# Kernel optimization log

Hardware: AMD Instinct MI355X
Metric: run time of the kernel (lower is better)

The kernel has to match this reference:

```python
import jax, jax.numpy as jnp
import numpy as np

DIM = 512
N_PATCH = 1024
HEADS = 8
LN_EPS = 1e-5
NORM_EPS = 1e-12


def _layernorm(x, g, b):
    mu = jnp.mean(x, axis=-1, keepdims=True)
    var = jnp.mean(jnp.square(x - mu), axis=-1, keepdims=True)
    return (x - mu) * jax.lax.rsqrt(var + LN_EPS) * g + b


def _l2norm(x):
    # matches F.normalize(dim=-1): x / max(||x||, eps)
    n = jnp.sqrt(jnp.sum(jnp.square(x), axis=-1, keepdims=True))
    return x / jnp.maximum(n, NORM_EPS)


def _gelu(x):
    return jax.nn.gelu(x, approximate=False)


def _cosine_attn_branch(x, qkv_w, qkv_b, ln_g, ln_b, proj_w, proj_b, temperature):
    B, N, D = x.shape
    H = HEADS
    hd = D // H
    qkv = _layernorm(x @ qkv_w + qkv_b, ln_g, ln_b)          # [B,N,3D]
    q, k, v = jnp.split(qkv, 3, axis=-1)
    def to_heads(t):
        return t.reshape(B, N, H, hd).transpose(0, 2, 1, 3)  # [B,H,N,hd]
    q, k, v = to_heads(q), to_heads(k), to_heads(v)
    q = _l2norm(q)
    k = _l2norm(k)
    # temperature: [H,1,1] broadcasts over [B,H,N,N]
    attn = jnp.einsum('bhnd,bhmd->bhnm', q, k) * temperature
    attn = jax.nn.softmax(attn, axis=-1)
    out = jnp.einsum('bhnm,bhmd->bhnd', attn, v)
    out = out.transpose(0, 2, 1, 3).reshape(B, N, D)
    return out @ proj_w + proj_b


def setup_inputs() -> dict:
    key = jax.random.key(0)
    ks = iter(jax.random.split(key, 40))
    D = DIM
    def rn(shape, scale=0.02):
        return (jax.random.normal(next(ks), shape, dtype=jnp.float32) * scale)
    inp = {
        'hsi_tokens': jax.random.normal(next(ks), (8, N_PATCH, D), dtype=jnp.float32),
        'lidar_tokens': jax.random.normal(next(ks), (8, N_PATCH, D), dtype=jnp.float32),
        'temperature': jnp.ones((HEADS, 1, 1), dtype=jnp.float32),
        'sq_w': rn((D, 3 * D)), 'sq_b': jnp.zeros((3 * D,), jnp.float32),
        'sq_ln_g': jnp.ones((3 * D,), jnp.float32), 'sq_ln_b': jnp.zeros((3 * D,), jnp.float32),
        'sproj_w': rn((D, D)), 'sproj_b': jnp.zeros((D,), jnp.float32),
        'pq_w': rn((D, 3 * D)), 'pq_b': jnp.zeros((3 * D,), jnp.float32),
        'pq_ln_g': jnp.ones((3 * D,), jnp.float32), 'pq_ln_b': jnp.zeros((3 * D,), jnp.float32),
        'pproj_w': rn((D, D)), 'pproj_b': jnp.zeros((D,), jnp.float32),
        'vf_w1': rn((D, 2 * D)), 'vf_b1': jnp.zeros((2 * D,), jnp.float32),
        'vf_w2': rn((2 * D, D)), 'vf_b2': jnp.zeros((D,), jnp.float32),
        'ag_w1': rn((2 * D, D)), 'ag_b1': jnp.zeros((D,), jnp.float32),
        'ag_ln_g': jnp.ones((D,), jnp.float32), 'ag_ln_b': jnp.zeros((D,), jnp.float32),
        'ag_w2': rn((D, 3)), 'ag_b2': jnp.zeros((3,), jnp.float32),
        'fr_w1': rn((D, 2 * D)), 'fr_b1': jnp.zeros((2 * D,), jnp.float32),
        'fr_w2': rn((2 * D, D)), 'fr_b2': jnp.zeros((D,), jnp.float32),
        'alpha': jnp.ones((1,), jnp.float32),
        'beta': jnp.ones((1,), jnp.float32),
    }
    return inp


def reference(hsi_tokens, lidar_tokens, temperature,
              sq_w, sq_b, sq_ln_g, sq_ln_b, sproj_w, sproj_b,
              pq_w, pq_b, pq_ln_g, pq_ln_b, pproj_w, pproj_b,
              vf_w1, vf_b1, vf_w2, vf_b2,
              ag_w1, ag_b1, ag_ln_g, ag_ln_b, ag_w2, ag_b2,
              fr_w1, fr_b1, fr_w2, fr_b2, alpha, beta):
    B, N, D = hsi_tokens.shape
    out_spectral = _cosine_attn_branch(hsi_tokens, sq_w, sq_b, sq_ln_g, sq_ln_b,
                                       sproj_w, sproj_b, temperature)
    out_spatial = _cosine_attn_branch(lidar_tokens, pq_w, pq_b, pq_ln_g, pq_ln_b,
                                      pproj_w, pproj_b, temperature)
    # volumetric fusion MLP (dropout is identity in eval)
    s = out_spectral + out_spatial
    volumetric_feat = _gelu(s @ vf_w1 + vf_b1) @ vf_w2 + vf_b2
    # adaptive gating
    hsi_global = jnp.mean(out_spectral, axis=1)    # [B,D]
    lidar_global = jnp.mean(out_spatial, axis=1)   # [B,D]
    concat = jnp.concatenate([hsi_global, lidar_global], axis=-1)  # [B,2D]
    g = _gelu(_layernorm(concat @ ag_w1 + ag_b1, ag_ln_g, ag_ln_b))
    gate = jax.nn.softmax(g @ ag_w2 + ag_b2, axis=-1)  # [B,3]
    w_spec = gate[:, 0][:, None, None]
    w_spat = gate[:, 1][:, None, None]
    w_vol = gate[:, 2][:, None, None]
    fused = w_spec * out_spectral + w_spat * out_spatial + w_vol * volumetric_feat
    fused_recal = _gelu(fused @ fr_w1 + fr_b1) @ fr_w2 + fr_b2
    return fused + alpha * fused_recal + beta * (hsi_tokens + lidar_tokens) * 0.5
```

## Files before the change

### kernel.cpp

```cpp
#include <hip/hip_runtime.h>
#include <hip/hip_bf16.h>
#include <math.h>

#define B_   8
#define N_   1024
#define D_   512
#define H_   8
#define HD_  64
#define D3_  1536
#define M_   (B_ * N_)

#define WOFF_SQ    0
#define WOFF_PQ    786432
#define WOFF_SPROJ 1572864
#define WOFF_PPROJ 1835008
#define WOFF_VF1   2097152
#define WOFF_VF2   2621440
#define WOFF_FR1   3145728
#define WOFF_FR2   3670016

typedef float f32x4 __attribute__((ext_vector_type(4)));
typedef __bf16 bf16x8 __attribute__((ext_vector_type(8)));

union FragU {
    uint4 u4;
    unsigned int u[4];
    ushort s[8];
    bf16x8 v;
};

static __device__ __forceinline__ ushort f2bf(float x) {
    union { __bf16 h; ushort u; } c;
    c.h = (__bf16)x;
    return c.u;
}

static __device__ __forceinline__ float bf2f(ushort u) {
    union { unsigned u; float f; } c;
    c.u = ((unsigned)u) << 16;
    return c.f;
}

static __device__ __forceinline__ unsigned int pack2(float a, float b) {
    return (unsigned int)f2bf(a) | ((unsigned int)f2bf(b) << 16);
}

static __device__ __forceinline__ float gelu_f(float x) {
    return 0.5f * x * (1.0f + erff(x * 0.7071067811865475f));
}

#if __has_builtin(__builtin_amdgcn_exp2f)
static __device__ __forceinline__ float exp2_fast(float x) { return __builtin_amdgcn_exp2f(x); }
#else
static __device__ __forceinline__ float exp2_fast(float x) { return exp2f(x); }
#endif

static __device__ __forceinline__ void gload16(const ushort* g, ushort* lds) {
    __builtin_amdgcn_global_load_lds(
        (const __attribute__((address_space(1))) void*)g,
        (__attribute__((address_space(3))) void*)lds, 16, 0, 0);
}

static __device__ __forceinline__ float blk_sum(float v, float* red) {
    #pragma unroll
    for (int off = 32; off; off >>= 1) v += __shfl_xor(v, off);
    const int w = threadIdx.x >> 6;
    __syncthreads();
    if ((threadIdx.x & 63) == 0) red[w] = v;
    __syncthreads();
    return red[0] + red[1] + red[2] + red[3];
}

template <int BM, int BN, int ACT, int OUT, bool FINAL, bool GROUP>
__global__ __launch_bounds__(256) void pgemm_k(
    const ushort* __restrict__ A, const ushort* __restrict__ Wt,
    const ushort* __restrict__ Wt2, const float* __restrict__ bias,
    const float* __restrict__ bias2, int Msplit,
    void* __restrict__ Cv, int nbx, int Nn, int K,
    const ushort* __restrict__ fusedb, const ushort* __restrict__ resb,
    const float* __restrict__ alphap, const float* __restrict__ betap)
{
    constexpr int MI = BM / 32;
    constexpr int NJ = BN / 32;
    constexpr int CA = BM / 16;
    constexpr int CB = BN / 16;
    __shared__ ushort Asm[2][BM * 32];
    __shared__ ushort Bsm[2][BN * 32];
    const int tid = threadIdx.x;
    const int w = tid >> 6, l = tid & 63;
    const int cpx = gridDim.x >> 3;
    const int wg = (blockIdx.x & 7) * cpx + (blockIdx.x >> 3);
    const int m0 = (wg / nbx) * BM, n0 = (wg % nbx) * BN;
    const int wr = w >> 1, wc = w & 1;
    const int lr = l & 15, g = l >> 4;

    const ushort* W_ = (!GROUP || m0 < Msplit) ? Wt : Wt2;
    const float* b_ = (!GROUP || m0 < Msplit) ? bias : bias2;

    f32x4 acc[MI][NJ] = {};
    const int nt = K >> 5;

    #define STAGE(buf, kt)                                                        \
        do {                                                                      \
            const int k0s = (kt) << 5;                                            \
            for (int c = w; c < CA; c += 4)                                       \
                gload16(&A[(size_t)(m0 + c * 16 + lr) * K + k0s + 8 * g],         \
                        &Asm[buf][c * 512]);                                      \
            for (int c = w; c < CB; c += 4)                                       \
                gload16(&W_[(size_t)(n0 + c * 16 + lr) * K + k0s + 8 * g],        \
                        &Bsm[buf][c * 512]);                                      \
        } while (0)

    STAGE(0, 0);
    __syncthreads();
    int cur = 0;
    for (int t = 0; t < nt; ++t) {
        if (t + 1 < nt) STAGE(cur ^ 1, t + 1);
        FragU af[MI], bf4[NJ];
        #pragma unroll
        for (int mi = 0; mi < MI; ++mi)
            af[mi].u4 = *reinterpret_cast<const uint4*>(
                &Asm[cur][(wr * MI + mi) * 512 + l * 8]);
        #pragma unroll
        for (int nj = 0; nj < NJ; ++nj)
            bf4[nj].u4 = *reinterpret_cast<const uint4*>(
                &Bsm[cur][(wc * NJ + nj) * 512 + l * 8]);
        #pragma unroll
        for (int mi = 0; mi < MI; ++mi)
            #pragma unroll
            for (int nj = 0; nj < NJ; ++nj)
                acc[mi][nj] = __builtin_amdgcn_mfma_f32_16x16x32_bf16(
                    af[mi].v, bf4[nj].v, acc[mi][nj], 0, 0, 0);
        __syncthreads();
        cur ^= 1;
    }
    #undef STAGE

    float alpha = 0.f, beta = 0.f;
    if (FINAL) { alpha = alphap[0]; beta = betap[0]; }
    #pragma unroll
    for (int mi = 0; mi < MI; ++mi) {
        #pragma unroll
        for (int r = 0; r < 4; ++r) {
            const int m = m0 + wr * (MI * 16) + mi * 16 + g * 4 + r;
            #pragma unroll
            for (int nj = 0; nj < NJ; ++nj) {
                const int n = n0 + wc * (NJ * 16) + nj * 16 + lr;
                const size_t idx = (size_t)m * Nn + n;
                float v = acc[mi][nj][r] + b_[n];
                if (ACT == 1) v = gelu_f(v);
                if (FINAL)
                    v = bf2f(fusedb[idx]) + alpha * v + beta * bf2f(resb[idx]);
                if (OUT == 0) ((float*)Cv)[idx] = v;
                else          ((ushort*)Cv)[idx] = f2bf(v);
            }
        }
    }
}

__global__ __launch_bounds__(256) void cvtw_k(
    const float* __restrict__ w0, const float* __restrict__ w1,
    const float* __restrict__ w2, const float* __restrict__ w3,
    const float* __restrict__ w4, const float* __restrict__ w5,
    const float* __restrict__ w6, const float* __restrict__ w7,
    ushort* __restrict__ dst)
{
    __shared__ ushort T[64][72];
    const int id = blockIdx.z;
    int K, Nn, off;
    const float* src;
    switch (id) {
        case 0: src = w0; K = 512;  Nn = 1536; off = WOFF_SQ;    break;
        case 1: src = w1; K = 512;  Nn = 1536; off = WOFF_PQ;    break;
        case 2: src = w2; K = 512;  Nn = 512;  off = WOFF_SPROJ; break;
        case 3: src = w3; K = 512;  Nn = 512;  off = WOFF_PPROJ; break;
        case 4: src = w4; K = 512;  Nn = 1024; off = WOFF_VF1;   break;
        case 5: src = w5; K = 1024; Nn = 512;  off = WOFF_VF2;   break;
        case 6: src = w6; K = 512;  Nn = 1024; off = WOFF_FR1;   break;
        default: src = w7; K = 1024; Nn = 512; off = WOFF_FR2;   break;
    }
    const int n0 = blockIdx.x * 64, k0 = blockIdx.y * 64;
    if (n0 >= Nn || k0 >= K) return;
    const int t = threadIdx.x;
    const int q = t >> 6, e = t & 63;
    #pragma unroll 4
    for (int i = 0; i < 16; ++i) {
        const int kl = q * 16 + i;
        T[e][kl] = f2bf(src[(size_t)(k0 + kl) * Nn + n0 + e]);
    }
    __syncthreads();
    #pragma unroll 4
    for (int i = 0; i < 16; ++i) {
        const int nl = q * 16 + i;
        dst[(size_t)off + (size_t)(n0 + nl) * K + k0 + e] = T[nl][e];
    }
}

__global__ __launch_bounds__(256) void cvt3_k(const float* __restrict__ h,
                                              const float* __restrict__ l,
                                              ushort* __restrict__ xh,
                                              ushort* __restrict__ xl,
                                              ushort* __restrict__ rb)
{
    const size_t i = ((size_t)blockIdx.x * 256 + threadIdx.x) * 8;
    const float4 h0 = *reinterpret_cast<const float4*>(h + i);
    const float4 h1 = *reinterpret_cast<const float4*>(h + i + 4);
    const float4 l0 = *reinterpret_cast<const float4*>(l + i);
    const float4 l1 = *reinterpret_cast<const float4*>(l + i + 4);
    FragU oh, ol, orr;
    oh.u[0] = pack2(h0.x, h0.y); oh.u[1] = pack2(h0.z, h0.w);
    oh.u[2] = pack2(h1.x, h1.y); oh.u[3] = pack2(h1.z, h1.w);
    ol.u[0] = pack2(l0.x, l0.y); ol.u[1] = pack2(l0.z, l0.w);
    ol.u[2] = pack2(l1.x, l1.y); ol.u[3] = pack2(l1.z, l1.w);
    orr.u[0] = pack2(0.5f * (h0.x + l0.x), 0.5f * (h0.y + l0.y));
    orr.u[1] = pack2(0.5f * (h0.z + l0.z), 0.5f * (h0.w + l0.w));
    orr.u[2] = pack2(0.5f * (h1.x + l1.x), 0.5f * (h1.y + l1.y));
    orr.u[3] = pack2(0.5f * (h1.z + l1.z), 0.5f * (h1.w + l1.w));
    *reinterpret_cast<uint4*>(xh + i) = oh.u4;
    *reinterpret_cast<uint4*>(xl + i) = ol.u4;
    *reinterpret_cast<uint4*>(rb + i) = orr.u4;
}

__global__ __launch_bounds__(256) void cvtadd_k(const ushort* __restrict__ a,
                                                const ushort* __restrict__ b,
                                                ushort* __restrict__ dst)
{
    const size_t i = ((size_t)blockIdx.x * 256 + threadIdx.x) * 8;
    FragU x, y, o;
    x.u4 = *reinterpret_cast<const uint4*>(a + i);
    y.u4 = *reinterpret_cast<const uint4*>(b + i);
    #pragma unroll
    for (int e = 0; e < 8; ++e) o.s[e] = f2bf(bf2f(x.s[e]) + bf2f(y.s[e]));
    *reinterpret_cast<uint4*>(dst + i) = o.u4;
}

__global__ __launch_bounds__(256) void lnprep_k(ushort* __restrict__ x,
                                                const float* __restrict__ lng0,
                                                const float* __restrict__ lnb0,
                                                const float* __restrict__ lng1,
                                                const float* __restrict__ lnb1,
                                                const float* __restrict__ temp,
                                                ushort* __restrict__ Kb,
                                                ushort* __restrict__ Vt)
{
    __shared__ ushort Vs[8 * 512];
    const int w = threadIdx.x >> 6, l = threadIdx.x & 63;
    const int n0 = blockIdx.x * 8;
    const float L2E = 1.4426950408889634f;
    const float* lng = (n0 < 8192) ? lng0 : lng1;
    const float* lnb = (n0 < 8192) ? lnb0 : lnb1;

    #pragma unroll
    for (int rr = 0; rr < 2; ++rr) {
        const int row = n0 + w * 2 + rr;
        const int bb = row >> 10;
        const int n = row & 1023;
        ushort* xr = x + (size_t)row * D3_;
        float qv[24];
        #pragma unroll
        for (int i = 0; i < 24; ++i) qv[i] = bf2f(xr[l + 64 * i]);
        float s = 0.f, ss = 0.f;
        #pragma unroll
        for (int i = 0; i < 24; ++i) { s += qv[i]; ss += qv[i] * qv[i]; }
        #pragma unroll
        for (int off = 32; off; off >>= 1) {
            s += __shfl_xor(s, off);
            ss += __shfl_xor(ss, off);
        }
        const float mu = s * (1.0f / D3_);
        const float var = ss * (1.0f / D3_) - mu * mu;
        const float rs = rsqrtf(var + 1e-5f);
        #pragma unroll
        for (int i = 0; i < 24; ++i)
            qv[i] = (qv[i] - mu) * rs * lng[l + 64 * i] + lnb[l + 64 * i];
        float sq[16];
        #pragma unroll
        for (int i = 0; i < 16; ++i) sq[i] = qv[i] * qv[i];
        #pragma unroll
        for (int off = 32; off; off >>= 1)
            #pragma unroll
            for (int i = 0; i < 16; ++i) sq[i] += __shfl_xor(sq[i], off);
        #pragma unroll
        for (int i = 0; i < 8; ++i) {
            const float qs = temp[i] * L2E / fmaxf(sqrtf(sq[i]), 1e-12f);
            xr[i * 64 + l] = f2bf(qv[i] * qs);
        }
        #pragma unroll
        for (int i = 0; i < 8; ++i) {
            const float ks = 1.0f / fmaxf(sqrtf(sq[8 + i]), 1e-12f);
            Kb[((size_t)(bb * 8 + i) * N_ + n) * HD_ + l] = f2bf(qv[8 + i] * ks);
        }
        #pragma unroll
        for (int i = 0; i < 8; ++i)
            Vs[(w * 2 + rr) * 512 + i * 64 + l] = f2bf(qv[16 + i]);
    }
    __syncthreads();
    const int bb = n0 >> 10;
    #pragma unroll
    for (int it = 0; it < 2; ++it) {
        const int combo = threadIdx.x + it * 256;
        FragU f;
        #pragma unroll
        for (int tok = 0; tok < 8; ++tok) f.s[tok] = Vs[tok * 512 + combo];
        *reinterpret_cast<uint4*>(
            &Vt[((size_t)(bb * 8 + (combo >> 6)) * HD_ + (combo & 63)) * N_ + (n0 & 1023)]) = f.u4;
    }
}

__global__ __launch_bounds__(256) void fattn_k(const ushort* __restrict__ Qu,
                                               const ushort* __restrict__ Kb,
                                               const ushort* __restrict__ Vt,
                                               const float* __restrict__ temp,
                                               ushort* __restrict__ out)
{
    __shared__ ushort Ks[2][64 * 72];
    __shared__ ushort Vs[2][64 * 72];
    const int tid = threadIdx.x;
    const int cpx = gridDim.x >> 3;
    const int wg = (blockIdx.x & 7) * cpx + (blockIdx.x >> 3);
    const int nb = wg & 7;
    const int h  = (wg >> 3) & 7;
    const int bb = wg >> 6;
    const int bh = bb * 8 + h;
    const int n0 = nb * 128;
    const int w  = tid >> 6;
    const int l  = tid & 63;
    const int lr = l & 15;
    const int g  = l >> 4;
    const float m2 = fabsf(temp[h]) * 1.4426950408889634f;
    const f32x4 mInit = {-m2, -m2, -m2, -m2};

    FragU ones;
    ones.u[0] = ones.u[1] = ones.u[2] = ones.u[3] = 0x3F803F80u;

    const int qb = n0 + w * 32;
    FragU qa0, qa1, qb0, qb1;
    {
        const size_t rb0 = (size_t)(bb * N_ + qb + lr) * D3_ + h * 64 + 8 * g;
        const size_t rb1 = (size_t)(bb * N_ + qb + 16 + lr) * D3_ + h * 64 + 8 * g;
        qa0.u4 = *reinterpret_cast<const uint4*>(&Qu[rb0]);
        qa1.u4 = *reinterpret_cast<const uint4*>(&Qu[rb0 + 32]);
        qb0.u4 = *reinterpret_cast<const uint4*>(&Qu[rb1]);
        qb1.u4 = *reinterpret_cast<const uint4*>(&Qu[rb1 + 32]);
    }

    f32x4 OA[4] = {};
    f32x4 OB[4] = {};
    f32x4 LSA = {0.f, 0.f, 0.f, 0.f};
    f32x4 LSB = {0.f, 0.f, 0.f, 0.f};

    const ushort* kbase = Kb + (size_t)bh * N_ * HD_;
    const ushort* vbase = Vt + (size_t)bh * HD_ * N_;
    const int sr = tid >> 3;
    const int sc = (tid & 7) * 8;
    uint4 k0r, k1r, v0r, v1r;

    #define LOADT(kt)                                                           \
        do {                                                                    \
            const ushort* ks_ = kbase + (size_t)((kt) * 64) * HD_;              \
            const ushort* vs_ = vbase + (kt) * 64;                              \
            k0r = *reinterpret_cast<const uint4*>(ks_ + sr * HD_ + sc);         \
            k1r = *reinterpret_cast<const uint4*>(ks_ + (sr + 32) * HD_ + sc);  \
            v0r = *reinterpret_cast<const uint4*>(vs_ + (size_t)sr * N_ + sc);  \
            v1r = *reinterpret_cast<const uint4*>(vs_ + (size_t)(sr + 32) * N_ + sc); \
        } while (0)
    #define WRITET(p)                                                           \
        do {                                                                    \
            *reinterpret_cast<uint4*>(&Ks[p][sr * 72 + sc]) = k0r;              \
            *reinterpret_cast<uint4*>(&Ks[p][(sr + 32) * 72 + sc]) = k1r;       \
            *reinterpret_cast<uint4*>(&Vs[p][sr * 72 + sc]) = v0r;              \
            *reinterpret_cast<uint4*>(&Vs[p][(sr + 32) * 72 + sc]) = v1r;       \
        } while (0)

    LOADT(0);
    WRITET(0);

    #pragma unroll 1
    for (int kt = 0; kt < 16; ++kt) {
        const int p = kt & 1;
        __syncthreads();
        if (kt < 15) LOADT(kt + 1);

        unsigned paA[2][4], paB[2][4];
        #pragma unroll
        for (int j = 0; j < 4; ++j) {
            FragU ka, kc;
            ka.u4 = *reinterpret_cast<const uint4*>(&Ks[p][(j * 16 + lr) * 72 + 8 * g]);
            kc.u4 = *reinterpret_cast<const uint4*>(&Ks[p][(j * 16 + lr) * 72 + 32 + 8 * g]);
            f32x4 sA = mInit, sB = mInit;
            sA = __builtin_amdgcn_mfma_f32_16x16x32_bf16(ka.v, qa0.v, sA, 0, 0, 0);
            sA = __builtin_amdgcn_mfma_f32_16x16x32_bf16(kc.v, qa1.v, sA, 0, 0, 0);
            sB = __builtin_amdgcn_mfma_f32_16x16x32_bf16(ka.v, qb0.v, sB, 0, 0, 0);
            sB = __builtin_amdgcn_mfma_f32_16x16x32_bf16(kc.v, qb1.v, sB, 0, 0, 0);
            float pA[4], pB[4];
            #pragma unroll
            for (int r = 0; r < 4; ++r) {
                pA[r] = exp2_fast(sA[r]);
                pB[r] = exp2_fast(sB[r]);
            }
            paA[j >> 1][2 * (j & 1) + 0] = pack2(pA[0], pA[1]);
            paA[j >> 1][2 * (j & 1) + 1] = pack2(pA[2], pA[3]);
            paB[j >> 1][2 * (j & 1) + 0] = pack2(pB[0], pB[1]);
            paB[j >> 1][2 * (j & 1) + 1] = pack2(pB[2], pB[3]);
        }

        __builtin_amdgcn_s_setprio(1);
        #pragma unroll
        for (int ks = 0; ks < 2; ++ks) {
            FragU fa, fb2;
            fa.u[0] = paA[ks][0]; fa.u[1] = paA[ks][1];
            fa.u[2] = paA[ks][2]; fa.u[3] = paA[ks][3];
            fb2.u[0] = paB[ks][0]; fb2.u[1] = paB[ks][1];
            fb2.u[2] = paB[ks][2]; fb2.u[3] = paB[ks][3];
            LSA = __builtin_amdgcn_mfma_f32_16x16x32_bf16(fa.v, ones.v, LSA, 0, 0, 0);
            LSB = __builtin_amdgcn_mfma_f32_16x16x32_bf16(fb2.v, ones.v, LSB, 0, 0, 0);
            #pragma unroll
            for (int s4 = 0; s4 < 4; ++s4) {
                FragU vb;
                const int vi = (lr + 16 * s4) * 72 + ks * 32 + 4 * g;
                *reinterpret_cast<uint2*>(&vb.u[0]) =
                    *reinterpret_cast<const uint2*>(&Vs[p][vi]);
                *reinterpret_cast<uint2*>(&vb.u[2]) =
                    *reinterpret_cast<const uint2*>(&Vs[p][vi + 16]);
                OA[s4] = __builtin_amdgcn_mfma_f32_16x16x32_bf16(fa.v, vb.v, OA[s4], 0, 0, 0);
                OB[s4] = __builtin_amdgcn_mfma_f32_16x16x32_bf16(fb2.v, vb.v, OB[s4], 0, 0, 0);
            }
        }
        __builtin_amdgcn_s_setprio(0);

        if (kt < 15) WRITET(p ^ 1);
    }
    #undef LOADT
    #undef WRITET

    ushort* outp = out + ((size_t)(bb * N_) + qb) * D_ + h * HD_;
    #pragma unroll
    for (int r = 0; r < 4; ++r) {
        const float iA = 1.0f / LSA[r];
        const float iB = 1.0f / LSB[r];
        ushort* rowA = outp + (size_t)(4 * g + r) * D_;
        ushort* rowB = outp + (size_t)(16 + 4 * g + r) * D_;
        #pragma unroll
        for (int s4 = 0; s4 < 4; ++s4) {
            rowA[s4 * 16 + lr] = f2bf(OA[s4][r] * iA);
            rowB[s4 * 16 + lr] = f2bf(OB[s4][r] * iB);
        }
    }
}

__global__ __launch_bounds__(256) void means_k(const ushort* __restrict__ spec,
                                               const ushort* __restrict__ spat,
                                               float* __restrict__ Gp)
{
    const int b = blockIdx.x >> 5;
    const int ch = blockIdx.x & 31;
    const int n0 = ch * 32;
    const int d0 = threadIdx.x * 2;
    float s1a = 0.f, s1b = 0.f, s2a = 0.f, s2b = 0.f;
    #pragma unroll 4
    for (int n = 0; n < 32; ++n) {
        const size_t idx = ((size_t)(b * N_) + n0 + n) * D_ + d0;
        ushort u1[2], u2[2];
        *reinterpret_cast<unsigned*>(u1) = *reinterpret_cast<const unsigned*>(spec + idx);
        *reinterpret_cast<unsigned*>(u2) = *reinterpret_cast<const unsigned*>(spat + idx);
        s1a += bf2f(u1[0]); s1b += bf2f(u1[1]);
        s2a += bf2f(u2[0]); s2b += bf2f(u2[1]);
    }
    float* gp = Gp + (size_t)blockIdx.x * 1024;
    gp[d0] = s1a; gp[d0 + 1] = s1b;
    gp[512 + d0] = s2a; gp[512 + d0 + 1] = s2b;
}

__global__ __launch_bounds__(256) void gate1_k(const float* __restrict__ Gp,
                                               const float* __restrict__ w1,
                                               const float* __restrict__ b1,
                                               float* __restrict__ y)
{
    __shared__ float xs[1024];
    __shared__ float red[4][64];
    const int jc = blockIdx.x, b = blockIdx.y, tid = threadIdx.x;
    for (int k = tid; k < 1024; k += 256) {
        float s = 0.f;
        #pragma unroll 8
        for (int c = 0; c < 32; ++c) s += Gp[(size_t)(b * 32 + c) * 1024 + k];
        xs[k] = s * (1.0f / N_);
    }
    __syncthreads();
    const int jl = tid & 63;
    const int jj = jc * 64 + jl;
    const int seg = tid >> 6;
    float acc = 0.f;
    const float* wp = w1 + (size_t)(seg * 256) * 512 + jj;
    const float* xp = xs + seg * 256;
    #pragma unroll 8
    for (int k = 0; k < 256; ++k) acc += xp[k] * wp[(size_t)k * 512];
    red[seg][jl] = acc;
    __syncthreads();
    if (tid < 64)
        y[b * 512 + jc * 64 + tid] =
            red[0][tid] + red[1][tid] + red[2][tid] + red[3][tid] + b1[jc * 64 + tid];
}

__global__ __launch_bounds__(256) void gate2_k(const float* __restrict__ y,
                                               const float* __restrict__ lng,
                                               const float* __restrict__ lnb,
                                               const float* __restrict__ w2,
                                               const float* __restrict__ b2,
                                               float* __restrict__ gate)
{
    __shared__ float red[4];
    const int b = blockIdx.x, tid = threadIdx.x;
    const float v0 = y[b * 512 + tid];
    const float v1 = y[b * 512 + 256 + tid];
    const float s = blk_sum(v0 + v1, red);
    const float ss = blk_sum(v0 * v0 + v1 * v1, red);
    const float mu = s * (1.0f / 512.0f);
    const float var = ss * (1.0f / 512.0f) - mu * mu;
    const float rs = rsqrtf(var + 1e-5f);
    const float z0 = gelu_f((v0 - mu) * rs * lng[tid] + lnb[tid]);
    const float z1 = gelu_f((v1 - mu) * rs * lng[tid + 256] + lnb[tid + 256]);
    float p0 = z0 * w2[tid * 3 + 0] + z1 * w2[(tid + 256) * 3 + 0];
    float p1 = z0 * w2[tid * 3 + 1] + z1 * w2[(tid + 256) * 3 + 1];
    float p2 = z0 * w2[tid * 3 + 2] + z1 * w2[(tid + 256) * 3 + 2];
    p0 = blk_sum(p0, red);
    p1 = blk_sum(p1, red);
    p2 = blk_sum(p2, red);
    if (tid == 0) {
        p0 += b2[0]; p1 += b2[1]; p2 += b2[2];
        const float m = fmaxf(p0, fmaxf(p1, p2));
        const float e0 = expf(p0 - m), e1 = expf(p1 - m), e2 = expf(p2 - m);
        const float inv = 1.0f / (e0 + e1 + e2);
        gate[b * 3 + 0] = e0 * inv;
        gate[b * 3 + 1] = e1 * inv;
        gate[b * 3 + 2] = e2 * inv;
    }
}

__global__ __launch_bounds__(256) void fuse_k(
    const ushort* __restrict__ spec, const ushort* __restrict__ spat,
    const ushort* __restrict__ volb, const float* __restrict__ gate,
    ushort* __restrict__ fb)
{
    const size_t i4 = ((size_t)blockIdx.x * 256 + threadIdx.x) * 4;
    const int b = (int)(i4 >> 19);
    const float g0 = gate[b * 3 + 0], g1 = gate[b * 3 + 1], g2 = gate[b * 3 + 2];
    ushort au[4], cu[4], vu[4];
    *reinterpret_cast<uint2*>(au) = *reinterpret_cast<const uint2*>(spec + i4);
    *reinterpret_cast<uint2*>(cu) = *reinterpret_cast<const uint2*>(spat + i4);
    *reinterpret_cast<uint2*>(vu) = *reinterpret_cast<const uint2*>(volb + i4);
    union { ushort s[4]; uint2 u; } ob;
    #pragma unroll
    for (int e = 0; e < 4; ++e)
        ob.s[e] = f2bf(g0 * bf2f(au[e]) + g1 * bf2f(cu[e]) + g2 * bf2f(vu[e]));
    *reinterpret_cast<uint2*>(fb + i4) = ob.u;
}

extern "C" void kernel_launch(void* const* d_in, const int* in_sizes, int n_in,
                              void* d_out, int out_size, void* d_ws, size_t ws_size,
                              hipStream_t stream)
{
    const float* hsi    = (const float*)d_in[0];
    const float* lidar  = (const float*)d_in[1];
    const float* temp   = (const float*)d_in[2];
    const float* sq_w   = (const float*)d_in[3];
    const float* sq_b   = (const float*)d_in[4];
    const float* sq_lng = (const float*)d_in[5];
    const float* sq_lnb = (const float*)d_in[6];
    const float* sproj_w = (const float*)d_in[7];
    const float* sproj_b = (const float*)d_in[8];
    const float* pq_w   = (const float*)d_in[9];
    const float* pq_b   = (const float*)d_in[10];
    const float* pq_lng = (const float*)d_in[11];
    const float* pq_lnb = (const float*)d_in[12];
    const float* pproj_w = (const float*)d_in[13];
    const float* pproj_b = (const float*)d_in[14];
    const float* vf_w1  = (const float*)d_in[15];
    const float* vf_b1  = (const float*)d_in[16];
    const float* vf_w2  = (const float*)d_in[17];
    const float* vf_b2  = (const float*)d_in[18];
    const float* ag_w1  = (const float*)d_in[19];
    const float* ag_b1  = (const float*)d_in[20];
    const float* ag_lng = (const float*)d_in[21];
    const float* ag_lnb = (const float*)d_in[22];
    const float* ag_w2  = (const float*)d_in[23];
    const float* ag_b2  = (const float*)d_in[24];
    const float* fr_w1  = (const float*)d_in[25];
    const float* fr_b1  = (const float*)d_in[26];
    const float* fr_w2  = (const float*)d_in[27];
    const float* fr_b2  = (const float*)d_in[28];
    const float* alpha  = (const float*)d_in[29];
    const float* beta   = (const float*)d_in[30];
    float* out = (float*)d_out;

    ushort* base = (ushort*)d_ws;
    ushort* Qkv  = base;
    ushort* Ob   = base;
    ushort* Sb   = base + 8388608;
    ushort* volb = base + 12582912;
    ushort* fb   = base + 16777216;
    float*  Gp   = (float*)(base + 20971520);
    float*  gate = Gp + 262144;
    float*  ybuf = gate + 64;
    ushort* Kb   = base + 25165824;
    ushort* Vt   = base + 33554432;
    ushort* Hb   = base + 25165824;
    ushort* Ab   = base + 41943040;
    ushort* Xb   = base + 41943040;
    ushort* Wb   = base + 50331648;
    ushort* Rb   = base + 54525952;

    const dim3 blk(256);

    cvtw_k<<<dim3(24, 16, 8), blk, 0, stream>>>(sq_w, pq_w, sproj_w, pproj_w,
                                                vf_w1, vf_w2, fr_w1, fr_w2, Wb);
    cvt3_k<<<2048, blk, 0, stream>>>(hsi, lidar, Xb, Xb + (size_t)M_ * D_, Rb);

    pgemm_k<128,128,0,1,false,true><<<1536, blk, 0, stream>>>(
        Xb, Wb + WOFF_SQ, Wb + WOFF_PQ, sq_b, pq_b, M_,
        Qkv, 12, D3_, D_, nullptr, nullptr, nullptr, nullptr);

    lnprep_k<<<2048, blk, 0, stream>>>(Qkv, sq_lng, sq_lnb, pq_lng, pq_lnb,
                                       temp, Kb, Vt);

    fattn_k<<<1024, blk, 0, stream>>>(Qkv, Kb, Vt, temp, Ab);

    pgemm_k<128,64,0,1,false,true><<<1024, blk, 0, stream>>>(
        Ab, Wb + WOFF_SPROJ, Wb + WOFF_PPROJ, sproj_b, pproj_b, M_,
        Ob, 8, D_, D_, nullptr, nullptr, nullptr, nullptr);

    const ushort* spec_b = Ob;
    const ushort* spat_b = Ob + (size_t)M_ * D_;

    means_k<<<256, blk, 0, stream>>>(spec_b, spat_b, Gp);
    gate1_k<<<dim3(8, 8), blk, 0, stream>>>(Gp, ag_w1, ag_b1, ybuf);
    gate2_k<<<B_, blk, 0, stream>>>(ybuf, ag_lng, ag_lnb, ag_w2, ag_b2, gate);

    cvtadd_k<<<2048, blk, 0, stream>>>(spec_b, spat_b, Sb);
    pgemm_k<128,64,1,1,false,false><<<1024, blk, 0, stream>>>(
        Sb, Wb + WOFF_VF1, nullptr, vf_b1, nullptr, 0,
        Hb, 16, 1024, D_, nullptr, nullptr, nullptr, nullptr);
    pgemm_k<128,64,0,1,false,false><<<512, blk, 0, stream>>>(
        Hb, Wb + WOFF_VF2, nullptr, vf_b2, nullptr, 0,
        volb, 8, D_, 1024, nullptr, nullptr, nullptr, nullptr);

    fuse_k<<<4096, blk, 0, stream>>>(spec_b, spat_b, volb, gate, fb);
    pgemm_k<128,64,1,1,false,false><<<1024, blk, 0, stream>>>(
        fb, Wb + WOFF_FR1, nullptr, fr_b1, nullptr, 0,
        Hb, 16, 1024, D_, nullptr, nullptr, nullptr, nullptr);
    pgemm_k<128,64,0,0,true,false><<<512, blk, 0, stream>>>(
        Hb, Wb + WOFF_FR2, nullptr, fr_b2, nullptr, 0,
        out, 8, D_, 1024, fb, Rb, alpha, beta);
}
```

Before: 350.2 us.

## Load K/V fragments directly from global in flash attention, enlarge QKV GEMM tile

The flash attention kernel no longer stages K and V tiles through double-buffered shared memory with barriers. Each wave now reads its MFMA operand fragments straight from global memory and relies on the L1/L2 caches for reuse across the four waves. This removes LDS traffic and __syncthreads, but the loads are no longer software-prefetched, so latency can be exposed and global/cache traffic rises. Separately, the QKV projection GEMM tile grows from 128 to 256 rows and the grid shrinks to match.

```diff
diff --git a/kernel.cpp b/kernel.cpp
--- a/kernel.cpp
+++ b/kernel.cpp
@@ -313,8 +313,6 @@
                                                const float* __restrict__ temp,
                                                ushort* __restrict__ out)
 {
-    __shared__ ushort Ks[2][64 * 72];
-    __shared__ ushort Vs[2][64 * 72];
     const int tid = threadIdx.x;
     const int cpx = gridDim.x >> 3;
     const int wg = (blockIdx.x & 7) * cpx + (blockIdx.x >> 3);
@@ -351,42 +349,16 @@
 
     const ushort* kbase = Kb + (size_t)bh * N_ * HD_;
     const ushort* vbase = Vt + (size_t)bh * HD_ * N_;
-    const int sr = tid >> 3;
-    const int sc = (tid & 7) * 8;
-    uint4 k0r, k1r, v0r, v1r;
-
-    #define LOADT(kt)                                                           \
-        do {                                                                    \
-            const ushort* ks_ = kbase + (size_t)((kt) * 64) * HD_;              \
-            const ushort* vs_ = vbase + (kt) * 64;                              \
-            k0r = *reinterpret_cast<const uint4*>(ks_ + sr * HD_ + sc);         \
-            k1r = *reinterpret_cast<const uint4*>(ks_ + (sr + 32) * HD_ + sc);  \
-            v0r = *reinterpret_cast<const uint4*>(vs_ + (size_t)sr * N_ + sc);  \
-            v1r = *reinterpret_cast<const uint4*>(vs_ + (size_t)(sr + 32) * N_ + sc); \
-        } while (0)
-    #define WRITET(p)                                                           \
-        do {                                                                    \
-            *reinterpret_cast<uint4*>(&Ks[p][sr * 72 + sc]) = k0r;              \
-            *reinterpret_cast<uint4*>(&Ks[p][(sr + 32) * 72 + sc]) = k1r;       \
-            *reinterpret_cast<uint4*>(&Vs[p][sr * 72 + sc]) = v0r;              \
-            *reinterpret_cast<uint4*>(&Vs[p][(sr + 32) * 72 + sc]) = v1r;       \
-        } while (0)
-
-    LOADT(0);
-    WRITET(0);
 
     #pragma unroll 1
     for (int kt = 0; kt < 16; ++kt) {
-        const int p = kt & 1;
-        __syncthreads();
-        if (kt < 15) LOADT(kt + 1);
-
         unsigned paA[2][4], paB[2][4];
         #pragma unroll
         for (int j = 0; j < 4; ++j) {
+            const ushort* krow = kbase + (size_t)(kt * 64 + j * 16 + lr) * HD_ + 8 * g;
             FragU ka, kc;
-            ka.u4 = *reinterpret_cast<const uint4*>(&Ks[p][(j * 16 + lr) * 72 + 8 * g]);
-            kc.u4 = *reinterpret_cast<const uint4*>(&Ks[p][(j * 16 + lr) * 72 + 32 + 8 * g]);
+            ka.u4 = *reinterpret_cast<const uint4*>(krow);
+            kc.u4 = *reinterpret_cast<const uint4*>(krow + 32);
             f32x4 sA = mInit, sB = mInit;
             sA = __builtin_amdgcn_mfma_f32_16x16x32_bf16(ka.v, qa0.v, sA, 0, 0, 0);
             sA = __builtin_amdgcn_mfma_f32_16x16x32_bf16(kc.v, qa1.v, sA, 0, 0, 0);
@@ -416,22 +388,19 @@
             LSB = __builtin_amdgcn_mfma_f32_16x16x32_bf16(fb2.v, ones.v, LSB, 0, 0, 0);
             #pragma unroll
             for (int s4 = 0; s4 < 4; ++s4) {
+                const ushort* vrow = vbase + (size_t)(lr + 16 * s4) * N_
+                                     + kt * 64 + ks * 32 + 4 * g;
                 FragU vb;
-                const int vi = (lr + 16 * s4) * 72 + ks * 32 + 4 * g;
                 *reinterpret_cast<uint2*>(&vb.u[0]) =
-                    *reinterpret_cast<const uint2*>(&Vs[p][vi]);
+                    *reinterpret_cast<const uint2*>(vrow);
                 *reinterpret_cast<uint2*>(&vb.u[2]) =
-                    *reinterpret_cast<const uint2*>(&Vs[p][vi + 16]);
+                    *reinterpret_cast<const uint2*>(vrow + 16);
                 OA[s4] = __builtin_amdgcn_mfma_f32_16x16x32_bf16(fa.v, vb.v, OA[s4], 0, 0, 0);
                 OB[s4] = __builtin_amdgcn_mfma_f32_16x16x32_bf16(fb2.v, vb.v, OB[s4], 0, 0, 0);
             }
         }
         __builtin_amdgcn_s_setprio(0);
-
-        if (kt < 15) WRITET(p ^ 1);
-    }
-    #undef LOADT
-    #undef WRITET
+    }
 
     ushort* outp = out + ((size_t)(bb * N_) + qb) * D_ + h * HD_;
     #pragma unroll
@@ -615,7 +584,7 @@
                                                 vf_w1, vf_w2, fr_w1, fr_w2, Wb);
     cvt3_k<<<2048, blk, 0, stream>>>(hsi, lidar, Xb, Xb + (size_t)M_ * D_, Rb);
 
-    pgemm_k<128,128,0,1,false,true><<<1536, blk, 0, stream>>>(
+    pgemm_k<256,128,0,1,false,true><<<768, blk, 0, stream>>>(
         Xb, Wb + WOFF_SQ, Wb + WOFF_PQ, sq_b, pq_b, M_,
         Qkv, 12, D3_, D_, nullptr, nullptr, nullptr, nullptr);
 
```

Measured after the change: 533.1 us. +52.2%, slower.
